# Optimization experiments

Measured on AMD Instinct MI355X. Metric: run time of the kernel, lower is better.

Reference implementation:

```python
import jax, jax.numpy as jnp
import numpy as np

N = 12288          # total points across all clouds in the batch
NUM_CLOUDS = 8     # number of point clouds (batch ids)
D_POS = 3          # 3D coordinates
K = 20             # neighbors per point (includes self, loop=True)


def setup_inputs() -> dict:
    key = jax.random.key(0)
    kx, kb = jax.random.split(key)
    x = jax.random.normal(kx, (N, D_POS), dtype=jnp.float32)
    # sorted batch vector with variable-size groups, as torch_cluster expects
    batch = jnp.sort(jax.random.randint(kb, (N,), 0, NUM_CLOUDS, dtype=jnp.int32))
    return {"x": x, "batch": batch, "k": K}


def reference(x, batch, k):
    # positions = x (d=None -> use all columns), cast to float as in the module
    pos = x.astype(jnp.float32)                       # [N, d]
    sq = jnp.sum(pos * pos, axis=1)                   # [N]
    # squared euclidean pairwise distances: [N, N]
    dist = sq[:, None] + sq[None, :] - 2.0 * (pos @ pos.T)
    # batch-aware masking: neighbors must come from the same cloud
    same_cloud = batch[:, None] == batch[None, :]     # [N, N] bool
    dist = jnp.where(same_cloud, dist, jnp.inf)
    # k smallest distances per row; loop=True so self (dist ~ 0) is included
    _, neighbor_indices = jax.lax.top_k(-dist, k)     # [N, k] int32
    return neighbor_indices
```

## Files before the change

kernel.cpp:

```cpp
#include <hip/hip_runtime.h>
#include <stdint.h>


#define MAXC 28
#define NCLOUDS 8
#define ROWS_PER_BLOCK 4
#define BIGF 3.0e38f

__device__ __forceinline__ unsigned int map32(float d) {
    unsigned int u = __float_as_uint(d);
    return u ^ (unsigned int)(((int)u >> 31) | 0x80000000);
}

__device__ __forceinline__ unsigned long long map64(double d) {
    unsigned long long u = __double_as_longlong(d);
    return u ^ (unsigned long long)(((long long)u >> 63) |
                                    (long long)0x8000000000000000ull);
}

__device__ __forceinline__ unsigned int umin2(unsigned int a, unsigned int b) {
    return a < b ? a : b;
}

__device__ __forceinline__ unsigned int wave_umin_dpp(unsigned int v) {
    int x = (int)v, t;
    t = __builtin_amdgcn_update_dpp(-1, x, 0x111, 0xf, 0xf, false);
    x = (int)umin2((unsigned int)x, (unsigned int)t);
    t = __builtin_amdgcn_update_dpp(-1, x, 0x112, 0xf, 0xf, false);
    x = (int)umin2((unsigned int)x, (unsigned int)t);
    t = __builtin_amdgcn_update_dpp(-1, x, 0x114, 0xf, 0xf, false);
    x = (int)umin2((unsigned int)x, (unsigned int)t);
    t = __builtin_amdgcn_update_dpp(-1, x, 0x118, 0xf, 0xf, false);
    x = (int)umin2((unsigned int)x, (unsigned int)t);
    t = __builtin_amdgcn_update_dpp(-1, x, 0x142, 0xa, 0xf, false);
    x = (int)umin2((unsigned int)x, (unsigned int)t);
    t = __builtin_amdgcn_update_dpp(-1, x, 0x143, 0xc, 0xf, false);
    x = (int)umin2((unsigned int)x, (unsigned int)t);
    return (unsigned int)__builtin_amdgcn_readlane(x, 63);
}

__global__ void bounds_kernel(const int* __restrict__ batch, int n,
                              int* __restrict__ starts, int* __restrict__ ends) {
    int j = blockIdx.x * blockDim.x + threadIdx.x;
    if (j >= n) return;
    int b = batch[j];
    if (b < 0 || b >= NCLOUDS) return;
    if (j == 0 || batch[j - 1] != b) starts[b] = j;
    if (j == n - 1 || batch[j + 1] != b) ends[b] = j + 1;
}

__global__ __launch_bounds__(256) void knn_main_kernel(
        const float* __restrict__ x,
        const int* __restrict__ batch,
        const int* __restrict__ starts,
        const int* __restrict__ ends,
        int k, int n,
        int* __restrict__ out) {
#pragma clang fp contract(off)
    __shared__ int coll[ROWS_PER_BLOCK][64];
    const int wave = threadIdx.x >> 6;
    const int lane = threadIdx.x & 63;
    const int i = blockIdx.x * ROWS_PER_BLOCK + wave;
    if (i >= n) return;

    const int b = batch[i];
    const int s0 = starts[b];
    const int e0 = ends[b];

    const float xi0 = x[3 * i + 0];
    const float xi1 = x[3 * i + 1];
    const float xi2 = x[3 * i + 2];
    const float sqi = xi0 * xi0 + xi1 * xi1 + xi2 * xi2;

    float slots[MAXC];
    float c0 = BIGF, c1 = BIGF, c2 = BIGF, c3 = BIGF;
#pragma unroll
    for (int t = 0; t < MAXC; ++t) {
        const int j = s0 + lane + t * 64;
        const int jc = (j < e0) ? j : (e0 - 1);
        const float y0 = x[3 * jc + 0];
        const float y1 = x[3 * jc + 1];
        const float y2 = x[3 * jc + 2];
        const float sqj = y0 * y0 + y1 * y1 + y2 * y2;
        float dot = __builtin_fmaf(xi2, y2,
                    __builtin_fmaf(xi1, y1, xi0 * y0));
        float s = sqi + sqj;
        float d = __builtin_fmaf(-2.0f, dot, s);
        d = (j < e0) ? d : BIGF;
        slots[t] = d;
        switch (t & 3) {
            case 0: c0 = fminf(c0, d); break;
            case 1: c1 = fminf(c1, d); break;
            case 2: c2 = fminf(c2, d); break;
            default: c3 = fminf(c3, d); break;
        }
    }
    const float localmin = fminf(fminf(c0, c1), fminf(c2, c3));

    float v = localmin;
#pragma unroll
    for (int kk = 2; kk <= 64; kk <<= 1) {
#pragma unroll
        for (int jj = kk >> 1; jj > 0; jj >>= 1) {
            float p = __int_as_float(__shfl_xor(__float_as_int(v), jj));
            bool keepMin = (((lane & jj) == 0) == ((lane & kk) == 0));
            v = keepMin ? fminf(v, p) : fmaxf(v, p);
        }
    }
    const float T = __int_as_float(
        __builtin_amdgcn_readlane(__float_as_int(v), k - 1));

    int base = 0;
#pragma unroll
    for (int t = 0; t < MAXC; ++t) {
        bool hit = (slots[t] <= T);
        unsigned long long bal = __ballot(hit);
        int off = base + __builtin_amdgcn_mbcnt_hi(
                             (unsigned int)(bal >> 32),
                             __builtin_amdgcn_mbcnt_lo((unsigned int)bal, 0));
        if (hit && off < 64) coll[wave][off] = lane + t * 64;
        base += (int)__popcll(bal);
    }

    if (base > 64) {
        unsigned int thrp1 = 0, Tu = 0;
        for (int r = 0; r < k; ++r) {
            unsigned int m0 = map32(slots[0]) - thrp1;
#pragma unroll
            for (int t = 1; t < MAXC; ++t)
                m0 = umin2(m0, map32(slots[t]) - thrp1);
            Tu = wave_umin_dpp(m0) + thrp1;
            thrp1 = Tu + 1;
        }
        base = 0;
#pragma unroll
        for (int t = 0; t < MAXC; ++t) {
            bool hit = (map32(slots[t]) <= Tu);
            unsigned long long bal = __ballot(hit);
            int off = base + __builtin_amdgcn_mbcnt_hi(
                                 (unsigned int)(bal >> 32),
                                 __builtin_amdgcn_mbcnt_lo((unsigned int)bal, 0));
            if (hit && off < 64) coll[wave][off] = lane + t * 64;
            base += (int)__popcll(bal);
        }
    }
    const int cnt = base < 64 ? base : 64;

    const bool valid = (lane < cnt);
    const int slot = valid ? coll[wave][lane] : 0;
    const int jc = s0 + slot;
    float v32 = BIGF;
    unsigned long long m64 = ~0ull;
    int oidx = 0;
    if (valid) {
        const float y0 = x[3 * jc + 0];
        const float y1 = x[3 * jc + 1];
        const float y2 = x[3 * jc + 2];
        oidx = jc;
        float dot = __builtin_fmaf(xi2, y2,
                    __builtin_fmaf(xi1, y1, xi0 * y0));
        float s = sqi + (y0 * y0 + y1 * y1 + y2 * y2);
        v32 = __builtin_fmaf(-2.0f, dot, s);
        double q0 = (double)xi0 * (double)xi0;
        double q1 = (double)xi1 * (double)xi1;
        double q2 = (double)xi2 * (double)xi2;
        double sqdi = (q0 + q1) + q2;
        double w0 = (double)y0 * (double)y0;
        double w1 = (double)y1 * (double)y1;
        double w2 = (double)y2 * (double)y2;
        double sqdj = (w0 + w1) + w2;
        double p0 = (double)xi0 * (double)y0;
        double p1 = (double)xi1 * (double)y1;
        double p2 = (double)xi2 * (double)y2;
        double dot64 = (p0 + p1) + p2;
        double d64 = (sqdi + sqdj) - 2.0 * dot64;
        m64 = map64(d64);
    }

    int pos = 0;
    for (int s = 0; s < cnt; ++s) {
        float vs = __int_as_float(__shfl(__float_as_int(v32), s));
        unsigned long long ms = __shfl(m64, s);
        int is_ = __shfl(oidx, s);
        bool less = (vs < v32) ||
                    (vs == v32 && (ms < m64 || (ms == m64 && is_ < oidx)));
        pos += less ? 1 : 0;
    }

    if (valid && pos < k) out[(long long)i * k + pos] = oidx;
}

extern "C" void kernel_launch(void* const* d_in, const int* in_sizes, int n_in,
                              void* d_out, int out_size, void* d_ws, size_t ws_size,
                              hipStream_t stream) {
    const float* x = (const float*)d_in[0];
    const int* batch = (const int*)d_in[1];
    const int n = in_sizes[1];
    const int k = out_size / n;
    int* out = (int*)d_out;

    int* starts = (int*)d_ws;
    int* ends = starts + NCLOUDS;

    bounds_kernel<<<(n + 255) / 256, 256, 0, stream>>>(batch, n, starts, ends);
    const int blocks = (n + ROWS_PER_BLOCK - 1) / ROWS_PER_BLOCK;
    knn_main_kernel<<<blocks, 256, 0, stream>>>(x, batch, starts, ends, k, n, out);
}
```

Before: 93.31 us.

## Pre-pack per-cloud padded float4 points with precomputed squared norms

Adds a scatter kernel that copies each cloud's points into a padded per-cloud float4 buffer holding x, y, z and the squared norm, with sentinel far points in the padding. The main kernel then does one vector load per candidate and drops the per-candidate norm computation, bounds clamp and mask select. The cost is an extra kernel launch and a workspace buffer. Correctness relies on each cloud fitting in the fixed padded capacity, and the sentinel distances must stay above any real distance.

```diff
diff --git a/kernel.cpp b/kernel.cpp
--- a/kernel.cpp
+++ b/kernel.cpp
@@ -3,6 +3,7 @@
 
 
 #define MAXC 28
+#define PADC 1792
 #define NCLOUDS 8
 #define ROWS_PER_BLOCK 4
 #define BIGF 3.0e38f
@@ -49,11 +50,34 @@
     if (j == n - 1 || batch[j + 1] != b) ends[b] = j + 1;
 }
 
+__global__ void scatter_kernel(const float* __restrict__ x, int n,
+                               const int* __restrict__ starts,
+                               const int* __restrict__ ends,
+                               float4* __restrict__ pts) {
+#pragma clang fp contract(off)
+    int p = blockIdx.x * blockDim.x + threadIdx.x;
+    if (p >= NCLOUDS * PADC) return;
+    int c = p / PADC;
+    int r = p - c * PADC;
+    int s = starts[c];
+    int e = ends[c];
+    bool ok = (s >= 0) && (e <= n) && (s < e);
+    int j = s + r;
+    if (ok && j < e) {
+        float x0 = x[3 * j + 0];
+        float x1 = x[3 * j + 1];
+        float x2 = x[3 * j + 2];
+        float sq = x0 * x0 + x1 * x1 + x2 * x2;
+        pts[p] = make_float4(x0, x1, x2, sq);
+    } else {
+        pts[p] = make_float4(1e18f, 1e18f, 1e18f, 3e36f);
+    }
+}
+
 __global__ __launch_bounds__(256) void knn_main_kernel(
-        const float* __restrict__ x,
+        const float4* __restrict__ pts,
         const int* __restrict__ batch,
         const int* __restrict__ starts,
-        const int* __restrict__ ends,
         int k, int n,
         int* __restrict__ out) {
 #pragma clang fp contract(off)
@@ -65,28 +89,18 @@
 
     const int b = batch[i];
     const int s0 = starts[b];
-    const int e0 = ends[b];
-
-    const float xi0 = x[3 * i + 0];
-    const float xi1 = x[3 * i + 1];
-    const float xi2 = x[3 * i + 2];
-    const float sqi = xi0 * xi0 + xi1 * xi1 + xi2 * xi2;
+    const int cbase = b * PADC;
+    const float4 q = pts[cbase + (i - s0)];
 
     float slots[MAXC];
     float c0 = BIGF, c1 = BIGF, c2 = BIGF, c3 = BIGF;
 #pragma unroll
     for (int t = 0; t < MAXC; ++t) {
-        const int j = s0 + lane + t * 64;
-        const int jc = (j < e0) ? j : (e0 - 1);
-        const float y0 = x[3 * jc + 0];
-        const float y1 = x[3 * jc + 1];
-        const float y2 = x[3 * jc + 2];
-        const float sqj = y0 * y0 + y1 * y1 + y2 * y2;
-        float dot = __builtin_fmaf(xi2, y2,
-                    __builtin_fmaf(xi1, y1, xi0 * y0));
-        float s = sqi + sqj;
+        const float4 wj = pts[cbase + lane + t * 64];
+        float dot = __builtin_fmaf(q.z, wj.z,
+                    __builtin_fmaf(q.y, wj.y, q.x * wj.x));
+        float s = q.w + wj.w;
         float d = __builtin_fmaf(-2.0f, dot, s);
-        d = (j < e0) ? d : BIGF;
         slots[t] = d;
         switch (t & 3) {
             case 0: c0 = fminf(c0, d); break;
@@ -148,30 +162,27 @@
 
     const bool valid = (lane < cnt);
     const int slot = valid ? coll[wave][lane] : 0;
-    const int jc = s0 + slot;
     float v32 = BIGF;
     unsigned long long m64 = ~0ull;
     int oidx = 0;
     if (valid) {
-        const float y0 = x[3 * jc + 0];
-        const float y1 = x[3 * jc + 1];
-        const float y2 = x[3 * jc + 2];
-        oidx = jc;
-        float dot = __builtin_fmaf(xi2, y2,
-                    __builtin_fmaf(xi1, y1, xi0 * y0));
-        float s = sqi + (y0 * y0 + y1 * y1 + y2 * y2);
+        const float4 wj = pts[cbase + slot];
+        oidx = s0 + slot;
+        float dot = __builtin_fmaf(q.z, wj.z,
+                    __builtin_fmaf(q.y, wj.y, q.x * wj.x));
+        float s = q.w + wj.w;
         v32 = __builtin_fmaf(-2.0f, dot, s);
-        double q0 = (double)xi0 * (double)xi0;
-        double q1 = (double)xi1 * (double)xi1;
-        double q2 = (double)xi2 * (double)xi2;
+        double q0 = (double)q.x * (double)q.x;
+        double q1 = (double)q.y * (double)q.y;
+        double q2 = (double)q.z * (double)q.z;
         double sqdi = (q0 + q1) + q2;
-        double w0 = (double)y0 * (double)y0;
-        double w1 = (double)y1 * (double)y1;
-        double w2 = (double)y2 * (double)y2;
+        double w0 = (double)wj.x * (double)wj.x;
+        double w1 = (double)wj.y * (double)wj.y;
+        double w2 = (double)wj.z * (double)wj.z;
         double sqdj = (w0 + w1) + w2;
-        double p0 = (double)xi0 * (double)y0;
-        double p1 = (double)xi1 * (double)y1;
-        double p2 = (double)xi2 * (double)y2;
+        double p0 = (double)q.x * (double)wj.x;
+        double p1 = (double)q.y * (double)wj.y;
+        double p2 = (double)q.z * (double)wj.z;
         double dot64 = (p0 + p1) + p2;
         double d64 = (sqdi + sqdj) - 2.0 * dot64;
         m64 = map64(d64);
@@ -199,10 +210,13 @@
     const int k = out_size / n;
     int* out = (int*)d_out;
 
-    int* starts = (int*)d_ws;
-    int* ends = starts + NCLOUDS;
+    char* ws = (char*)d_ws;
+    float4* pts = (float4*)ws;            ws += (size_t)NCLOUDS * PADC * sizeof(float4);
+    int* starts = (int*)ws;               ws += NCLOUDS * sizeof(int);
+    int* ends = (int*)ws;
 
     bounds_kernel<<<(n + 255) / 256, 256, 0, stream>>>(batch, n, starts, ends);
+    scatter_kernel<<<(NCLOUDS * PADC + 255) / 256, 256, 0, stream>>>(x, n, starts, ends, pts);
     const int blocks = (n + ROWS_PER_BLOCK - 1) / ROWS_PER_BLOCK;
-    knn_main_kernel<<<blocks, 256, 0, stream>>>(x, batch, starts, ends, k, n, out);
-}
+    knn_main_kernel<<<blocks, 256, 0, stream>>>(pts, batch, starts, k, n, out);
+}
```

Result: faster. 91.14 us (-2.3%).
